# Optimization experiments

Measured on AMD Instinct MI355X. Metric: run time of the kernel, lower is better.

The kernel has to match this reference:

```python
import jax, jax.numpy as jnp
import numpy as np

ALPHA = 0.3
TEMPERATURE = 2.0
LN_EPS = 1e-5
NORM_EPS = 1e-8


def setup_inputs() -> dict:
    key = jax.random.key(0)
    k1, k2 = jax.random.split(key)
    B, N, D = 2, 4096, 512
    F = D // 2 + 1  # rfft output bins = 257
    x = jax.random.normal(k1, (B, N, D), dtype=jnp.float32)
    # spectral_proj: Linear(F, F, bias=False); kaiming-uniform-ish scale
    W_spec = jax.random.normal(k2, (F, F), dtype=jnp.float32) * (1.0 / np.sqrt(F))
    gamma = jnp.ones((D,), dtype=jnp.float32)   # LayerNorm weight
    beta = jnp.zeros((D,), dtype=jnp.float32)   # LayerNorm bias
    return {"x": x, "W_spec": W_spec, "gamma": gamma, "beta": beta}


def reference(x, W_spec, gamma, beta):
    # x: (B, N, D) real
    x_hat = jnp.fft.rfft(x, axis=-1)                       # (B, N, F) complex64
    # complex input through real-weight linear: x_hat @ W^T
    x_hat = jnp.einsum('bnf,gf->bng', x_hat, W_spec.astype(x_hat.dtype))
    # complex magnitude normalization per token
    norms = jnp.sqrt(jnp.sum(jnp.abs(x_hat) ** 2, axis=-1, keepdims=True) + NORM_EPS)
    x_norm = x_hat / norms                                 # (B, N, F) complex
    # spectral correlation: |x_norm @ x_norm^H|
    S = jnp.abs(jnp.einsum('bnf,bmf->bnm', x_norm, jnp.conj(x_norm)))  # (B, N, N) real
    S_soft = jax.nn.softmax(S / TEMPERATURE, axis=-1)      # dropout is identity (eval)
    mixed = jnp.einsum('bnm,bmd->bnd', S_soft, x)          # (B, N, D)
    h = x + ALPHA * (mixed - x)                            # residual blend
    # LayerNorm over last dim
    mu = jnp.mean(h, axis=-1, keepdims=True)
    var = jnp.mean((h - mu) ** 2, axis=-1, keepdims=True)
    out = (h - mu) / jnp.sqrt(var + LN_EPS) * gamma + beta
    return out, S
```

## Files before the change

kernel.cpp:

```cpp
#include <hip/hip_runtime.h>
#include <hip/hip_bf16.h>
#include <math.h>

#define BB 2
#define NN 4096
#define DD 512
#define FF 257
#define FP 288
#define KK2 (2*FP)
#define NT 528
#define PI_F 3.14159265358979323846f

typedef __attribute__((ext_vector_type(4))) float f32x4;
typedef __attribute__((ext_vector_type(8))) short bf16x8;
typedef unsigned int u32;
typedef unsigned short u16;

#define MT_OFF  0u
#define XF_OFF  1052672u
#define SS_OFF  10489856u
#define NR_OFF  (SS_OFF + 8388608u)
#define XT_OFF  77598720u
#define MX_OFF  85987328u

#define AS1 __attribute__((address_space(1)))
#define AS3 __attribute__((address_space(3)))

static __device__ __forceinline__ void gl2lds(const u16* g, u16* l) {
    __builtin_amdgcn_global_load_lds((const AS1 u32*)(unsigned long long)g,
                                     (AS3 u32*)(unsigned)(unsigned long long)l,
                                     16, 0, 0);
}

static __device__ __forceinline__ unsigned short f2bf(float f) {
    unsigned int u = __float_as_uint(f);
    unsigned int r = (u + 0x7fffu + ((u >> 16) & 1u)) >> 16;
    return (unsigned short)r;
}
static __device__ __forceinline__ float bf2f(unsigned short s) {
    return __uint_as_float(((unsigned int)s) << 16);
}

static __device__ __forceinline__ bf16x8 conj_swap(bf16x8 a) {
    union { bf16x8 v; u32 u[4]; } s, d;
    s.v = a;
#pragma unroll
    for (int i = 0; i < 4; ++i) {
        u32 w = s.u[i];
        d.u[i] = ((w >> 16) | (w << 16)) ^ 0x80000000u;
    }
    return d.v;
}

__global__ __launch_bounds__(256) void k_zero(float* __restrict__ norms,
                                              u16* __restrict__ Mt) {
    int i = blockIdx.x * 256 + threadIdx.x;
    if (i < 8192) norms[i] = 0.f;
    Mt[514 * 512 + i] = 0;
}

__global__ __launch_bounds__(512) void k_build_Mt(const float* __restrict__ W,
                                                  u16* __restrict__ Mt) {
    __shared__ float twr[512], twi[512], wrow[FF];
    const int g = blockIdx.x;
    const int d = threadIdx.x;
    {
        float s, c;
        sincosf(-(2.0f * PI_F / 512.0f) * (float)d, &s, &c);
        twr[d] = c; twi[d] = s;
    }
    for (int f = d; f < FF; f += 512) wrow[f] = W[g * FF + f];
    __syncthreads();
    float re = 0.f, im = 0.f;
    for (int f = 0; f < FF; ++f) {
        float w = wrow[f];
        int k = (f * d) & 511;
        re = fmaf(w, twr[k], re);
        im = fmaf(w, twi[k], im);
    }
    Mt[(size_t)(2 * g) * 512 + d]     = f2bf(re);
    Mt[(size_t)(2 * g + 1) * 512 + d] = f2bf(im);
}

__global__ __launch_bounds__(256) void k_xcast(const float* __restrict__ x,
                                               u16* __restrict__ xb) {
    const size_t i = ((size_t)blockIdx.x * 256 + threadIdx.x) * 8;
    float4 a = *(const float4*)(x + i);
    float4 b = *(const float4*)(x + i + 4);
    union { u16 h[8]; uint4 q; } o;
    o.h[0] = f2bf(a.x); o.h[1] = f2bf(a.y); o.h[2] = f2bf(a.z); o.h[3] = f2bf(a.w);
    o.h[4] = f2bf(b.x); o.h[5] = f2bf(b.y); o.h[6] = f2bf(b.z); o.h[7] = f2bf(b.w);
    *(uint4*)(xb + i) = o.q;
}

__global__ __launch_bounds__(256) void k_proj_mfma(const u16* __restrict__ xb,
                                                   const u16* __restrict__ Mt,
                                                   u16* __restrict__ xhat,
                                                   float* __restrict__ norms) {
    __shared__ u16 As[128 * 64];
    __shared__ u16 Bs[64 * 64];
    const int prow = blockIdx.y * 128;
    const int gcol = blockIdx.x * 64;
    const int tid = threadIdx.x;
    const int lane = tid & 63;
    const int wave = tid >> 6;
    const int wr = wave * 32;
    const int fr = lane & 15;
    const int q  = lane >> 4;
    const int sw = lane & 7;

    const u16* __restrict__ Arow = xb + (size_t)prow * DD;
    const u16* __restrict__ Brow = Mt + (size_t)gcol * DD;

    const int cs0 = (q ^ sw) * 8;
    const int cs1 = ((4 + q) ^ sw) * 8;

    f32x4 acc[2][4];
#pragma unroll
    for (int m = 0; m < 2; ++m)
#pragma unroll
        for (int n = 0; n < 4; ++n) acc[m][n] = (f32x4)0.f;

    int rA[2], rB[4];
#pragma unroll
    for (int m = 0; m < 2; ++m) rA[m] = (wr + m * 16 + fr) * 64;
#pragma unroll
    for (int n = 0; n < 4; ++n) rB[n] = (n * 16 + fr) * 64;

    for (int kc = 0; kc < DD / 64; ++kc) {
        const int k0 = kc * 64;
        __syncthreads();
#pragma unroll
        for (int it = 0; it < 4; ++it) {
            int e = tid + it * 256;
            int row = e >> 3, ch = e & 7;
            gl2lds(Arow + (size_t)row * DD + k0 + (ch ^ (row & 7)) * 8, &As[e * 8]);
        }
#pragma unroll
        for (int it = 0; it < 2; ++it) {
            int e = tid + it * 256;
            int row = e >> 3, ch = e & 7;
            gl2lds(Brow + (size_t)row * DD + k0 + (ch ^ (row & 7)) * 8, &Bs[e * 8]);
        }
        __syncthreads();
#pragma unroll
        for (int kk = 0; kk < 2; ++kk) {
            const int cs = kk ? cs1 : cs0;
            bf16x8 av[2], bv[4];
#pragma unroll
            for (int m = 0; m < 2; ++m) av[m] = *(const bf16x8*)&As[rA[m] + cs];
#pragma unroll
            for (int n = 0; n < 4; ++n) bv[n] = *(const bf16x8*)&Bs[rB[n] + cs];
#pragma unroll
            for (int m = 0; m < 2; ++m)
#pragma unroll
                for (int n = 0; n < 4; ++n)
                    acc[m][n] = __builtin_amdgcn_mfma_f32_16x16x32_bf16(av[m], bv[n], acc[m][n], 0, 0, 0);
        }
    }

#pragma unroll
    for (int m = 0; m < 2; ++m) {
#pragma unroll
        for (int reg = 0; reg < 4; ++reg) {
            const int r = prow + wr + m * 16 + q * 4 + reg;
            u16* __restrict__ rp = xhat + (size_t)r * KK2 + gcol + fr;
            float sq = 0.f;
#pragma unroll
            for (int n = 0; n < 4; ++n) {
                float v = acc[m][n][reg];
                rp[n * 16] = f2bf(v);
                sq = fmaf(v, v, sq);
            }
            sq += __shfl_xor(sq, 1);
            sq += __shfl_xor(sq, 2);
            sq += __shfl_xor(sq, 4);
            sq += __shfl_xor(sq, 8);
            if (fr == 0) atomicAdd(&norms[r], sq);
        }
    }
}

__global__ __launch_bounds__(256) void k_normalize(u32* __restrict__ Xf,
                                                   const float* __restrict__ norms) {
    const int row = blockIdx.x * 8 + (threadIdx.x >> 5);
    const int l = threadIdx.x & 31;
    const float rn = rsqrtf(norms[row] + 1e-8f);
    u32* __restrict__ p = Xf + (size_t)row * FP;
#pragma unroll
    for (int u = 0; u < 9; ++u) {
        u32 w = p[u * 32 + l];
        float lo = bf2f((u16)(w & 0xffffu)) * rn;
        float hi = bf2f((u16)(w >> 16)) * rn;
        p[u * 32 + l] = (u32)f2bf(lo) | ((u32)f2bf(hi) << 16);
    }
}

__global__ __launch_bounds__(256) void k_gram_mfma(const u16* __restrict__ Xf,
                                                   float* __restrict__ Sout) {
    __shared__ u16 Af[128 * 64];
    __shared__ u16 Bf[128 * 64];
    __shared__ float trs[32][129];
    int i = (int)blockIdx.x;
    int b = 0;
    if (i >= NT) { b = 1; i -= NT; }
    int a = 0;
    while (i >= 32 - a) { i -= 32 - a; ++a; }
    const int brow = a * 128;
    const int bcol = (a + i) * 128;

    const int tid = threadIdx.x;
    const int lane = tid & 63;
    const int wave = tid >> 6;
    const int wr = (wave >> 1) * 64;
    const int wc = (wave & 1) * 64;
    const int fr = lane & 15;
    const int q  = lane >> 4;
    const int sw = lane & 7;

    const u16* __restrict__ Arow = Xf + (size_t)(b * NN + brow) * KK2;
    const u16* __restrict__ Brow = Xf + (size_t)(b * NN + bcol) * KK2;

    int srow[4], soff[4];
#pragma unroll
    for (int it = 0; it < 4; ++it) {
        int e = tid + it * 256;
        int row = e >> 3, ch = e & 7;
        srow[it] = row;
        soff[it] = (ch ^ (row & 7)) * 8;
    }
    const int cs0 = (q ^ sw) * 8;
    const int cs1 = ((4 + q) ^ sw) * 8;

    f32x4 acc_re[4][4], acc_im[4][4];
#pragma unroll
    for (int m = 0; m < 4; ++m)
#pragma unroll
        for (int n = 0; n < 4; ++n) {
            acc_re[m][n] = (f32x4)0.f;
            acc_im[m][n] = (f32x4)0.f;
        }

    int rA[4], rB[4];
#pragma unroll
    for (int m = 0; m < 4; ++m) rA[m] = (wr + m * 16 + fr) * 64;
#pragma unroll
    for (int n = 0; n < 4; ++n) rB[n] = (wc + n * 16 + fr) * 64;

    for (int kc = 0; kc < KK2 / 64; ++kc) {
        const int k0 = kc * 64;
        __syncthreads();
#pragma unroll
        for (int it = 0; it < 4; ++it) {
            int e = tid + it * 256;
            gl2lds(Arow + (size_t)srow[it] * KK2 + k0 + soff[it], &Af[e * 8]);
            gl2lds(Brow + (size_t)srow[it] * KK2 + k0 + soff[it], &Bf[e * 8]);
        }
        __syncthreads();
#pragma unroll
        for (int kk = 0; kk < 2; ++kk) {
            const int cs = kk ? cs1 : cs0;
            bf16x8 av[4], bv[4], gv[4];
#pragma unroll
            for (int m = 0; m < 4; ++m) av[m] = *(const bf16x8*)&Af[rA[m] + cs];
#pragma unroll
            for (int n = 0; n < 4; ++n) bv[n] = *(const bf16x8*)&Bf[rB[n] + cs];
#pragma unroll
            for (int m = 0; m < 4; ++m) gv[m] = conj_swap(av[m]);
#pragma unroll
            for (int m = 0; m < 4; ++m)
#pragma unroll
                for (int n = 0; n < 4; ++n) {
                    acc_re[m][n] = __builtin_amdgcn_mfma_f32_16x16x32_bf16(av[m], bv[n], acc_re[m][n], 0, 0, 0);
                    acc_im[m][n] = __builtin_amdgcn_mfma_f32_16x16x32_bf16(gv[m], bv[n], acc_im[m][n], 0, 0, 0);
                }
        }
    }

    float* __restrict__ Sb = Sout + (size_t)b * NN * NN;
#pragma unroll
    for (int m = 0; m < 4; ++m) {
#pragma unroll
        for (int reg = 0; reg < 4; ++reg) {
            int r = brow + wr + m * 16 + q * 4 + reg;
            float* __restrict__ rp = Sb + (size_t)r * NN + bcol + wc + fr;
#pragma unroll
            for (int n = 0; n < 4; ++n) {
                float re = acc_re[m][n][reg], im = acc_im[m][n][reg];
                rp[n * 16] = sqrtf(fmaf(re, re, im * im));
            }
        }
    }
    if (brow == bcol) return;

#pragma unroll
    for (int p = 0; p < 4; ++p) {
        __syncthreads();
        if ((wave >> 1) == (p >> 1)) {
            const int mbase = (p & 1) * 2;
#pragma unroll
            for (int mm = 0; mm < 2; ++mm) {
                const int m = mbase + mm;
                const int i0 = mm * 16 + q * 4;
#pragma unroll
                for (int reg = 0; reg < 4; ++reg) {
#pragma unroll
                    for (int n = 0; n < 4; ++n) {
                        float re = acc_re[m][n][reg], im = acc_im[m][n][reg];
                        trs[i0 + reg][wc + n * 16 + fr] = sqrtf(fmaf(re, re, im * im));
                    }
                }
            }
        }
        __syncthreads();
        const int j0 = (tid & 7) * 4;
#pragma unroll
        for (int u = 0; u < 4; ++u) {
            const int mr = u * 32 + (tid >> 3);
            float4 v;
            v.x = trs[j0 + 0][mr];
            v.y = trs[j0 + 1][mr];
            v.z = trs[j0 + 2][mr];
            v.w = trs[j0 + 3][mr];
            *(float4*)(Sb + (size_t)(bcol + mr) * NN + brow + p * 32 + j0) = v;
        }
    }
}

__global__ __launch_bounds__(256) void k_softmax(const float* __restrict__ S,
                                                 unsigned short* __restrict__ Wout) {
    __shared__ float red[8];
    const size_t row = blockIdx.x;
    const int tid = threadIdx.x;
    const float4* __restrict__ p4 = (const float4*)(S + row * NN);
    float4 v[4];
    float vmax = -1e30f;
#pragma unroll
    for (int u = 0; u < 4; ++u) {
        v[u] = p4[u * 256 + tid];
        vmax = fmaxf(vmax, fmaxf(fmaxf(v[u].x, v[u].y), fmaxf(v[u].z, v[u].w)));
    }
    for (int off = 32; off > 0; off >>= 1) vmax = fmaxf(vmax, __shfl_down(vmax, off, 64));
    if ((tid & 63) == 0) red[tid >> 6] = vmax;
    __syncthreads();
    const float bmax = fmaxf(fmaxf(red[0], red[1]), fmaxf(red[2], red[3]));
    float s = 0.f;
#pragma unroll
    for (int u = 0; u < 4; ++u) {
        v[u].x = __expf((v[u].x - bmax) * 0.5f);
        v[u].y = __expf((v[u].y - bmax) * 0.5f);
        v[u].z = __expf((v[u].z - bmax) * 0.5f);
        v[u].w = __expf((v[u].w - bmax) * 0.5f);
        s += (v[u].x + v[u].y) + (v[u].z + v[u].w);
    }
    for (int off = 32; off > 0; off >>= 1) s += __shfl_down(s, off, 64);
    if ((tid & 63) == 0) red[4 + (tid >> 6)] = s;
    __syncthreads();
    const float rinv = 1.0f / ((red[4] + red[5]) + (red[6] + red[7]));
    ushort4* __restrict__ o4 = (ushort4*)(Wout + row * NN);
#pragma unroll
    for (int u = 0; u < 4; ++u) {
        ushort4 w;
        w.x = f2bf(v[u].x * rinv);
        w.y = f2bf(v[u].y * rinv);
        w.z = f2bf(v[u].z * rinv);
        w.w = f2bf(v[u].w * rinv);
        o4[u * 256 + tid] = w;
    }
}

__global__ __launch_bounds__(256) void k_xpose(const float* __restrict__ x,
                                               u16* __restrict__ xbT) {
    __shared__ u16 st[64][72];
    const int b = blockIdx.z;
    const int t0 = blockIdx.x * 64;
    const int d0 = blockIdx.y * 64;
    const int tid = threadIdx.x;
#pragma unroll
    for (int u = 0; u < 4; ++u) {
        int idx = tid + u * 256;
        int tl = idx >> 4, d4 = (idx & 15) * 4;
        float4 v = *(const float4*)(x + ((size_t)(b * NN) + t0 + tl) * DD + d0 + d4);
        st[tl][d4 + 0] = f2bf(v.x);
        st[tl][d4 + 1] = f2bf(v.y);
        st[tl][d4 + 2] = f2bf(v.z);
        st[tl][d4 + 3] = f2bf(v.w);
    }
    __syncthreads();
#pragma unroll
    for (int u = 0; u < 2; ++u) {
        int e = tid + u * 256;
        int dl = e >> 3, t8 = (e & 7) * 8;
        union { u16 h[8]; uint4 q; } o;
#pragma unroll
        for (int j = 0; j < 8; ++j) o.h[j] = st[t8 + j][dl];
        *(uint4*)(xbT + ((size_t)(b * DD) + d0 + dl) * NN + t0 + t8) = o.q;
    }
}

__global__ __launch_bounds__(256) void k_mixed_mfma(const u16* __restrict__ Ws,
                                                    const u16* __restrict__ xbT,
                                                    float* __restrict__ mixed) {
    __shared__ u16 As[64 * 64];
    __shared__ u16 Bs[128 * 64];
    const int b = blockIdx.z;
    const int brow = blockIdx.y * 64;
    const int bcol = blockIdx.x * 128;
    const int tid = threadIdx.x;
    const int lane = tid & 63;
    const int wave = tid >> 6;
    const int wr = (wave >> 1) * 32;
    const int wc = (wave & 1) * 64;
    const int fr = lane & 15;
    const int q  = lane >> 4;
    const int sw = lane & 7;

    const u16* __restrict__ Arow = Ws + (size_t)(b * NN + brow) * NN;
    const u16* __restrict__ Brow = xbT + ((size_t)(b * DD) + bcol) * NN;

    const int cs0 = (q ^ sw) * 8;
    const int cs1 = ((4 + q) ^ sw) * 8;

    f32x4 acc[2][4];
#pragma unroll
    for (int m = 0; m < 2; ++m)
#pragma unroll
        for (int n = 0; n < 4; ++n) acc[m][n] = (f32x4)0.f;

    int rA[2], rB[4];
#pragma unroll
    for (int m = 0; m < 2; ++m) rA[m] = (wr + m * 16 + fr) * 64;
#pragma unroll
    for (int n = 0; n < 4; ++n) rB[n] = (wc + n * 16 + fr) * 64;

    for (int kc = 0; kc < NN / 64; ++kc) {
        const int k0 = kc * 64;
        __syncthreads();
#pragma unroll
        for (int it = 0; it < 2; ++it) {
            int e = tid + it * 256;
            int row = e >> 3, ch = e & 7;
            gl2lds(Arow + (size_t)row * NN + k0 + (ch ^ (row & 7)) * 8, &As[e * 8]);
        }
#pragma unroll
        for (int it = 0; it < 4; ++it) {
            int e = tid + it * 256;
            int row = e >> 3, ch = e & 7;
            gl2lds(Brow + (size_t)row * NN + k0 + (ch ^ (row & 7)) * 8, &Bs[e * 8]);
        }
        __syncthreads();
#pragma unroll
        for (int kk = 0; kk < 2; ++kk) {
            const int cs = kk ? cs1 : cs0;
            bf16x8 av[2], bv[4];
#pragma unroll
            for (int m = 0; m < 2; ++m) av[m] = *(const bf16x8*)&As[rA[m] + cs];
#pragma unroll
            for (int n = 0; n < 4; ++n) bv[n] = *(const bf16x8*)&Bs[rB[n] + cs];
#pragma unroll
            for (int m = 0; m < 2; ++m)
#pragma unroll
                for (int n = 0; n < 4; ++n)
                    acc[m][n] = __builtin_amdgcn_mfma_f32_16x16x32_bf16(av[m], bv[n], acc[m][n], 0, 0, 0);
        }
    }

    float* __restrict__ ob = mixed + (size_t)b * NN * DD;
#pragma unroll
    for (int m = 0; m < 2; ++m) {
#pragma unroll
        for (int reg = 0; reg < 4; ++reg) {
            int r = brow + wr + m * 16 + q * 4 + reg;
            float* __restrict__ rp = ob + (size_t)r * DD + bcol + wc + fr;
#pragma unroll
            for (int n = 0; n < 4; ++n) rp[n * 16] = acc[m][n][reg];
        }
    }
}

__global__ __launch_bounds__(256) void k_ln(const float* __restrict__ x,
                                            const float* __restrict__ mixed,
                                            const float* __restrict__ gamma,
                                            const float* __restrict__ beta,
                                            float* __restrict__ out) {
    __shared__ float red[8];
    const size_t row = blockIdx.x;
    const int tid = threadIdx.x;
    const float* __restrict__ xr = x + row * DD;
    const float* __restrict__ mr = mixed + row * DD;
    float x0 = xr[tid], x1 = xr[tid + 256];
    float h0 = fmaf(0.3f, mr[tid] - x0, x0);
    float h1 = fmaf(0.3f, mr[tid + 256] - x1, x1);
    float s = h0 + h1;
    float sq = fmaf(h0, h0, h1 * h1);
    for (int off = 32; off > 0; off >>= 1) {
        s += __shfl_down(s, off, 64);
        sq += __shfl_down(sq, off, 64);
    }
    if ((tid & 63) == 0) { red[tid >> 6] = s; red[4 + (tid >> 6)] = sq; }
    __syncthreads();
    const float mu = ((red[0] + red[1]) + (red[2] + red[3])) * (1.0f / DD);
    const float var = ((red[4] + red[5]) + (red[6] + red[7])) * (1.0f / DD) - mu * mu;
    const float rstd = rsqrtf(var + 1e-5f);
    out[row * DD + tid] = fmaf((h0 - mu) * rstd, gamma[tid], beta[tid]);
    out[row * DD + tid + 256] = fmaf((h1 - mu) * rstd, gamma[tid + 256], beta[tid + 256]);
}

extern "C" void kernel_launch(void* const* d_in, const int* in_sizes, int n_in,
                              void* d_out, int out_size, void* d_ws, size_t ws_size,
                              hipStream_t stream) {
    const float* x     = (const float*)d_in[0];
    const float* Wspec = (const float*)d_in[1];
    const float* gamma = (const float*)d_in[2];
    const float* beta  = (const float*)d_in[3];
    float* out  = (float*)d_out;
    float* Sout = out + (size_t)BB * NN * DD;

    char* ws = (char*)d_ws;
    u16*   Mt    = (u16*)(ws + MT_OFF);
    u16*   Xf    = (u16*)(ws + XF_OFF);
    u32*   XfW   = (u32*)(ws + XF_OFF);
    u16*   xb    = (u16*)(ws + SS_OFF);
    float* norms = (float*)(ws + NR_OFF);
    u16*   Ssoft = (u16*)(ws + SS_OFF);
    u16*   xbT   = (u16*)(ws + XT_OFF);
    float* mixed = (float*)(ws + MX_OFF);

    hipLaunchKernelGGL(k_zero, dim3(124), dim3(256), 0, stream, norms, Mt);
    hipLaunchKernelGGL(k_build_Mt, dim3(257), dim3(512), 0, stream, Wspec, Mt);
    hipLaunchKernelGGL(k_xcast, dim3(2048), dim3(256), 0, stream, x, xb);
    hipLaunchKernelGGL(k_proj_mfma, dim3(KK2 / 64, (BB * NN) / 128), dim3(256), 0, stream,
                       xb, Mt, Xf, norms);
    hipLaunchKernelGGL(k_normalize, dim3(BB * NN / 8), dim3(256), 0, stream, XfW, norms);
    hipLaunchKernelGGL(k_gram_mfma, dim3(BB * NT), dim3(256), 0, stream, Xf, Sout);
    hipLaunchKernelGGL(k_softmax, dim3(BB * NN), dim3(256), 0, stream, Sout, Ssoft);
    hipLaunchKernelGGL(k_xpose, dim3(NN / 64, DD / 64, BB), dim3(256), 0, stream, x, xbT);
    hipLaunchKernelGGL(k_mixed_mfma, dim3(DD / 128, NN / 64, BB), dim3(256), 0, stream, Ssoft, xbT, mixed);
    hipLaunchKernelGGL(k_ln, dim3(BB * NN), dim3(256), 0, stream, x, mixed, gamma, beta, out);
}
```

Before: 386.5 us.

## Split-K mixed GEMM with atomics, single-pass softmax, and shared LDS in gram

The S·x GEMM is split four ways along K. Partial tiles are accumulated into a zeroed fp32 buffer with atomicAdd, which raises the block count from 512 to 2048 to improve CU occupancy. The softmax drops the max-subtraction pass and computes exp2 directly, since S is a magnitude of normalized vectors bounded by 1, removing one reduction and one barrier. The gram kernel aliases its transpose scratch onto the A/B tile LDS to reduce shared memory use. The cost is atomic traffic plus an extra memset, and the fp32 accumulation order is no longer deterministic.

```diff
diff --git a/kernel.cpp b/kernel.cpp
--- a/kernel.cpp
+++ b/kernel.cpp
@@ -9,7 +9,9 @@
 #define FP 288
 #define KK2 (2*FP)
 #define NT 528
+#define KS 4
 #define PI_F 3.14159265358979323846f
+#define CEXP 0.72134752044f
 
 typedef __attribute__((ext_vector_type(4))) float f32x4;
 typedef __attribute__((ext_vector_type(8))) short bf16x8;
@@ -22,6 +24,7 @@
 #define NR_OFF  (SS_OFF + 8388608u)
 #define XT_OFF  77598720u
 #define MX_OFF  85987328u
+#define MX_BYTES 16777216u
 
 #define AS1 __attribute__((address_space(1)))
 #define AS3 __attribute__((address_space(3)))
@@ -198,9 +201,11 @@
 
 __global__ __launch_bounds__(256) void k_gram_mfma(const u16* __restrict__ Xf,
                                                    float* __restrict__ Sout) {
-    __shared__ u16 Af[128 * 64];
-    __shared__ u16 Bf[128 * 64];
-    __shared__ float trs[32][129];
+    __shared__ __align__(16) char gsm[32768];
+    u16* Af = (u16*)gsm;
+    u16* Bf = (u16*)(gsm + 16384);
+    float (*trs)[129] = (float (*)[129])gsm;
+
     int i = (int)blockIdx.x;
     int b = 0;
     if (i >= NT) { b = 1; i -= NT; }
@@ -329,34 +334,25 @@
 
 __global__ __launch_bounds__(256) void k_softmax(const float* __restrict__ S,
                                                  unsigned short* __restrict__ Wout) {
-    __shared__ float red[8];
+    __shared__ float red[4];
     const size_t row = blockIdx.x;
     const int tid = threadIdx.x;
     const float4* __restrict__ p4 = (const float4*)(S + row * NN);
     float4 v[4];
-    float vmax = -1e30f;
+    float s = 0.f;
 #pragma unroll
     for (int u = 0; u < 4; ++u) {
         v[u] = p4[u * 256 + tid];
-        vmax = fmaxf(vmax, fmaxf(fmaxf(v[u].x, v[u].y), fmaxf(v[u].z, v[u].w)));
-    }
-    for (int off = 32; off > 0; off >>= 1) vmax = fmaxf(vmax, __shfl_down(vmax, off, 64));
-    if ((tid & 63) == 0) red[tid >> 6] = vmax;
+        v[u].x = exp2f(v[u].x * CEXP);
+        v[u].y = exp2f(v[u].y * CEXP);
+        v[u].z = exp2f(v[u].z * CEXP);
+        v[u].w = exp2f(v[u].w * CEXP);
+        s += (v[u].x + v[u].y) + (v[u].z + v[u].w);
+    }
+    for (int off = 32; off > 0; off >>= 1) s += __shfl_down(s, off, 64);
+    if ((tid & 63) == 0) red[tid >> 6] = s;
     __syncthreads();
-    const float bmax = fmaxf(fmaxf(red[0], red[1]), fmaxf(red[2], red[3]));
-    float s = 0.f;
-#pragma unroll
-    for (int u = 0; u < 4; ++u) {
-        v[u].x = __expf((v[u].x - bmax) * 0.5f);
-        v[u].y = __expf((v[u].y - bmax) * 0.5f);
-        v[u].z = __expf((v[u].z - bmax) * 0.5f);
-        v[u].w = __expf((v[u].w - bmax) * 0.5f);
-        s += (v[u].x + v[u].y) + (v[u].z + v[u].w);
-    }
-    for (int off = 32; off > 0; off >>= 1) s += __shfl_down(s, off, 64);
-    if ((tid & 63) == 0) red[4 + (tid >> 6)] = s;
-    __syncthreads();
-    const float rinv = 1.0f / ((red[4] + red[5]) + (red[6] + red[7]));
+    const float rinv = 1.0f / ((red[0] + red[1]) + (red[2] + red[3]));
     ushort4* __restrict__ o4 = (ushort4*)(Wout + row * NN);
 #pragma unroll
     for (int u = 0; u < 4; ++u) {
@@ -398,14 +394,16 @@
     }
 }
 
-__global__ __launch_bounds__(256) void k_mixed_mfma(const u16* __restrict__ Ws,
-                                                    const u16* __restrict__ xbT,
-                                                    float* __restrict__ mixed) {
+__global__ __launch_bounds__(256) void k_mixed_split(const u16* __restrict__ Ws,
+                                                     const u16* __restrict__ xbT,
+                                                     float* __restrict__ mixed) {
     __shared__ u16 As[64 * 64];
     __shared__ u16 Bs[128 * 64];
     const int b = blockIdx.z;
+    const int n4 = blockIdx.x & 3;
+    const int ks = blockIdx.x >> 2;
     const int brow = blockIdx.y * 64;
-    const int bcol = blockIdx.x * 128;
+    const int bcol = n4 * 128;
     const int tid = threadIdx.x;
     const int lane = tid & 63;
     const int wave = tid >> 6;
@@ -433,7 +431,9 @@
 #pragma unroll
     for (int n = 0; n < 4; ++n) rB[n] = (wc + n * 16 + fr) * 64;
 
-    for (int kc = 0; kc < NN / 64; ++kc) {
+    const int kc0 = ks * (NN / 64 / KS);
+    const int kc1 = kc0 + (NN / 64 / KS);
+    for (int kc = kc0; kc < kc1; ++kc) {
         const int k0 = kc * 64;
         __syncthreads();
 #pragma unroll
@@ -473,7 +473,7 @@
             int r = brow + wr + m * 16 + q * 4 + reg;
             float* __restrict__ rp = ob + (size_t)r * DD + bcol + wc + fr;
 #pragma unroll
-            for (int n = 0; n < 4; ++n) rp[n * 16] = acc[m][n][reg];
+            for (int n = 0; n < 4; ++n) atomicAdd(&rp[n * 16], acc[m][n][reg]);
         }
     }
 }
@@ -527,6 +527,7 @@
     float* mixed = (float*)(ws + MX_OFF);
 
     hipLaunchKernelGGL(k_zero, dim3(124), dim3(256), 0, stream, norms, Mt);
+    hipMemsetAsync(mixed, 0, MX_BYTES, stream);
     hipLaunchKernelGGL(k_build_Mt, dim3(257), dim3(512), 0, stream, Wspec, Mt);
     hipLaunchKernelGGL(k_xcast, dim3(2048), dim3(256), 0, stream, x, xb);
     hipLaunchKernelGGL(k_proj_mfma, dim3(KK2 / 64, (BB * NN) / 128), dim3(256), 0, stream,
@@ -535,6 +536,7 @@
     hipLaunchKernelGGL(k_gram_mfma, dim3(BB * NT), dim3(256), 0, stream, Xf, Sout);
     hipLaunchKernelGGL(k_softmax, dim3(BB * NN), dim3(256), 0, stream, Sout, Ssoft);
     hipLaunchKernelGGL(k_xpose, dim3(NN / 64, DD / 64, BB), dim3(256), 0, stream, x, xbT);
-    hipLaunchKernelGGL(k_mixed_mfma, dim3(DD / 128, NN / 64, BB), dim3(256), 0, stream, Ssoft, xbT, mixed);
+    hipLaunchKernelGGL(k_mixed_split, dim3((DD / 128) * KS, NN / 64, BB), dim3(256), 0, stream,
+                       Ssoft, xbT, mixed);
     hipLaunchKernelGGL(k_ln, dim3(BB * NN), dim3(256), 0, stream, x, mixed, gamma, beta, out);
 }
```

Measured after the change: 413.1 us. +6.9%, slower.
